# Kernel tuning notes

Measured on AMD Instinct MI355X. Metric: run time of the kernel, lower is better.

The kernel has to match this reference:

```python
import jax, jax.numpy as jnp
import numpy as np

E, T, H, I = 32, 512, 2048, 768


def setup_inputs() -> dict:
    key = jax.random.key(0)
    k1, k2, k3, k4 = jax.random.split(key, 4)
    scale = 1.0 / np.sqrt(H)
    return {
        "routed_input": jax.random.normal(k1, (E, T, H), dtype=jnp.float32),
        "gate_proj": jax.random.normal(k2, (E, I, H), dtype=jnp.float32) * scale,
        "up_proj": jax.random.normal(k3, (E, I, H), dtype=jnp.float32) * scale,
        "down_proj": jax.random.normal(k4, (E, H, I), dtype=jnp.float32) * scale,
    }


def reference(routed_input, gate_proj, up_proj, down_proj):
    # routed_input: [E, T, H]; per-expert SwiGLU MLP, concat over experts.
    gate = jnp.einsum("eth,eih->eti", routed_input, gate_proj)
    up = jnp.einsum("eth,eih->eti", routed_input, up_proj)
    hidden = jax.nn.silu(gate) * up  # [E, T, I]
    out = jnp.einsum("eti,ehi->eth", hidden, down_proj)  # [E, T, H]
    return out.reshape(E * T, H)
```

## Files before the change

kernel.cpp:

```cpp
#include <hip/hip_runtime.h>


#define NE 32
#define NT 512
#define NH 2048
#define NI 768

typedef short        short8  __attribute__((ext_vector_type(8)));
typedef float        floatx4 __attribute__((ext_vector_type(4)));
typedef __attribute__((address_space(1))) const unsigned int g_u32;
typedef __attribute__((address_space(3))) unsigned int l_u32;

__device__ __forceinline__ void gl_lds16(const void* g, void* l) {
    __builtin_amdgcn_global_load_lds((g_u32*)g, (l_u32*)l, 16, 0, 0);
}

__device__ __forceinline__ unsigned int cvt_pk_bf16(float lo, float hi) {
    unsigned int r;
    asm("v_cvt_pk_bf16_f32 %0, %1, %2" : "=v"(r) : "v"(lo), "v"(hi));
    return r;
}

__device__ __forceinline__ short8 frag8(floatx4 x0, floatx4 x1) {
    union { unsigned int u[4]; short8 s; } t;
    t.u[0] = cvt_pk_bf16(x0[0], x0[1]);
    t.u[1] = cvt_pk_bf16(x0[2], x0[3]);
    t.u[2] = cvt_pk_bf16(x1[0], x1[1]);
    t.u[3] = cvt_pk_bf16(x1[2], x1[3]);
    return t.s;
}

__device__ __forceinline__ ushort f2bf(float f) {
    union { float f; unsigned int u; } v; v.f = f;
    unsigned int r = v.u + 0x7fffu + ((v.u >> 16) & 1u);
    return (ushort)(r >> 16);
}

__global__ __launch_bounds__(256, 2) void moe_gateup(
    const float* __restrict__ rin, const float* __restrict__ gate,
    const float* __restrict__ up, ushort* __restrict__ hidden)
{
    __shared__ float As[128][32];
    __shared__ float Gs[128][32];
    __shared__ float Us[128][32];

    const int bid = blockIdx.x;
    const int wg  = (bid & 7) * (768 / 8) + (bid >> 3);
    const int e   = wg / 24;
    const int rem = wg % 24;
    const int ti  = rem % 6;
    const int tm  = rem / 6;

    const int tid  = threadIdx.x;
    const int lane = tid & 63;
    const int wave = tid >> 6;
    const int wr = wave >> 1, wc = wave & 1;

    const float* Ab = rin  + (size_t)e * NT * NH + (size_t)(tm * 128) * NH;
    const float* Gb = gate + (size_t)e * NI * NH + (size_t)(ti * 128) * NH;
    const float* Ub = up   + (size_t)e * NI * NH + (size_t)(ti * 128) * NH;

    const int lr = lane >> 3;
    const int lc = lane & 7;

    floatx4 accg[4][4], accu[4][4];
    #pragma unroll
    for (int m = 0; m < 4; ++m)
        #pragma unroll
        for (int n = 0; n < 4; ++n) {
            accg[m][n] = (floatx4)0.f;
            accu[m][n] = (floatx4)0.f;
        }

    const int frow = lane & 15;
    const int h    = lane >> 4;
    const int rb   = frow & 7;
    const int c0   = (2 * h) ^ rb;
    const int c1   = (2 * h + 1) ^ rb;
    const int KT = NH / 32;

    for (int kt = 0; kt < KT; ++kt) {
        const int k0 = kt * 32;
        __builtin_amdgcn_s_barrier();
        #pragma unroll
        for (int i = 0; i < 4; ++i) {
            const int g = wave * 4 + i;
            const int r = g * 8 + lr;
            const int cs = lc ^ (r & 7);
            const size_t so = (size_t)r * NH + k0 + cs * 4;
            gl_lds16(Ab + so, &As[g * 8][0]);
            gl_lds16(Gb + so, &Gs[g * 8][0]);
            gl_lds16(Ub + so, &Us[g * 8][0]);
        }
        asm volatile("s_waitcnt vmcnt(0)" ::: "memory");
        __builtin_amdgcn_s_barrier();

        short8 af[4], gf[4], uf[4];
        #pragma unroll
        for (int m = 0; m < 4; ++m) {
            const int R = wr * 64 + m * 16 + frow;
            af[m] = frag8(*(const floatx4*)&As[R][c0 * 4],
                          *(const floatx4*)&As[R][c1 * 4]);
        }
        #pragma unroll
        for (int n = 0; n < 4; ++n) {
            const int R = wc * 64 + n * 16 + frow;
            gf[n] = frag8(*(const floatx4*)&Gs[R][c0 * 4],
                          *(const floatx4*)&Gs[R][c1 * 4]);
            uf[n] = frag8(*(const floatx4*)&Us[R][c0 * 4],
                          *(const floatx4*)&Us[R][c1 * 4]);
        }
        #pragma unroll
        for (int m = 0; m < 4; ++m)
            #pragma unroll
            for (int n = 0; n < 4; ++n) {
                accg[m][n] = __builtin_amdgcn_mfma_f32_16x16x32_bf16(
                    af[m], gf[n], accg[m][n], 0, 0, 0);
                accu[m][n] = __builtin_amdgcn_mfma_f32_16x16x32_bf16(
                    af[m], uf[n], accu[m][n], 0, 0, 0);
            }
    }

    const int ccol  = lane & 15;
    const int crow0 = (lane >> 4) * 4;
    const size_t hbase = ((size_t)e * NT + (size_t)tm * 128) * NI + ti * 128;
    #pragma unroll
    for (int m = 0; m < 4; ++m)
        #pragma unroll
        for (int n = 0; n < 4; ++n)
            #pragma unroll
            for (int j = 0; j < 4; ++j) {
                const float g = accg[m][n][j];
                const float u = accu[m][n][j];
                const float hh = (g / (1.f + __expf(-g))) * u;
                const int row = wr * 64 + m * 16 + crow0 + j;
                const int col = wc * 64 + n * 16 + ccol;
                hidden[hbase + (size_t)row * NI + col] = f2bf(hh);
            }
}

__global__ __launch_bounds__(256, 2) void moe_down(
    const ushort* __restrict__ hidden, const float* __restrict__ down,
    float* __restrict__ out)
{
    __shared__ ushort As[128][32];
    __shared__ float  Bs[128][32];

    const int bid = blockIdx.x;
    const int wg  = (bid & 7) * (2048 / 8) + (bid >> 3);
    const int e   = wg >> 6;
    const int rem = wg & 63;
    const int tn  = rem & 15;
    const int tm  = rem >> 4;

    const int tid  = threadIdx.x;
    const int lane = tid & 63;
    const int wave = tid >> 6;
    const int wr = wave >> 1, wc = wave & 1;

    const ushort* Ab = hidden + ((size_t)e * NT + (size_t)tm * 128) * NI;
    const float*  Bb = down + (size_t)e * NH * NI + (size_t)(tn * 128) * NI;

    floatx4 acc[4][4];
    #pragma unroll
    for (int m = 0; m < 4; ++m)
        #pragma unroll
        for (int n = 0; n < 4; ++n) acc[m][n] = (floatx4)0.f;

    const int frow = lane & 15;
    const int h    = lane >> 4;
    const int ca   = h ^ (frow & 3);
    const int rb   = frow & 7;
    const int c0   = (2 * h) ^ rb;
    const int c1   = (2 * h + 1) ^ rb;
    const int KT = NI / 32;

    for (int kt = 0; kt < KT; ++kt) {
        const int k0 = kt * 32;
        __builtin_amdgcn_s_barrier();
        #pragma unroll
        for (int i = 0; i < 2; ++i) {
            const int g = wave * 2 + i;
            const int r = g * 16 + (lane >> 2);
            const int cs = (lane & 3) ^ (r & 3);
            gl_lds16(Ab + (size_t)r * NI + k0 + cs * 8, &As[g * 16][0]);
        }
        #pragma unroll
        for (int i = 0; i < 4; ++i) {
            const int g = wave * 4 + i;
            const int r = g * 8 + (lane >> 3);
            const int cs = (lane & 7) ^ (r & 7);
            gl_lds16(Bb + (size_t)r * NI + k0 + cs * 4, &Bs[g * 8][0]);
        }
        asm volatile("s_waitcnt vmcnt(0)" ::: "memory");
        __builtin_amdgcn_s_barrier();

        short8 af[4], bf[4];
        #pragma unroll
        for (int m = 0; m < 4; ++m) {
            const int R = wr * 64 + m * 16 + frow;
            af[m] = *(const short8*)&As[R][ca * 8];
        }
        #pragma unroll
        for (int n = 0; n < 4; ++n) {
            const int R = wc * 64 + n * 16 + frow;
            bf[n] = frag8(*(const floatx4*)&Bs[R][c0 * 4],
                          *(const floatx4*)&Bs[R][c1 * 4]);
        }
        #pragma unroll
        for (int m = 0; m < 4; ++m)
            #pragma unroll
            for (int n = 0; n < 4; ++n)
                acc[m][n] = __builtin_amdgcn_mfma_f32_16x16x32_bf16(
                    af[m], bf[n], acc[m][n], 0, 0, 0);
    }

    const int ccol  = lane & 15;
    const int crow0 = (lane >> 4) * 4;
    float* Ob = out + ((size_t)e * NT + (size_t)tm * 128) * NH + tn * 128;
    #pragma unroll
    for (int m = 0; m < 4; ++m)
        #pragma unroll
        for (int n = 0; n < 4; ++n)
            #pragma unroll
            for (int j = 0; j < 4; ++j) {
                const int row = wr * 64 + m * 16 + crow0 + j;
                const int col = wc * 64 + n * 16 + ccol;
                Ob[(size_t)row * NH + col] = acc[m][n][j];
            }
}

extern "C" void kernel_launch(void* const* d_in, const int* in_sizes, int n_in,
                              void* d_out, int out_size, void* d_ws, size_t ws_size,
                              hipStream_t stream) {
    const float* rin  = (const float*)d_in[0];
    const float* gate = (const float*)d_in[1];
    const float* up   = (const float*)d_in[2];
    const float* down = (const float*)d_in[3];
    float* out = (float*)d_out;
    ushort* hidden = (ushort*)d_ws;

    dim3 blk(256);
    moe_gateup<<<dim3(768), blk, 0, stream>>>(rin, gate, up, hidden);
    moe_down<<<dim3(2048), blk, 0, stream>>>(hidden, down, out);
}
```

Before: 384.0 us.

## Double-buffer LDS tiles in gate/up and down GEMM kernels

Both GEMM kernels now keep two LDS buffers and issue the global-to-LDS loads for the next K tile before computing on the current one. They wait only for the older batch with a partial vmcnt and add a trailing barrier so the buffer being refilled is no longer being read. The aim is to hide global load latency behind MFMA work instead of fully serialising load and compute. In exchange, LDS use doubles (96KB for gate/up), and gate/up's launch bound drops to one block per CU, which lowers occupancy.

```diff
diff --git a/kernel.cpp b/kernel.cpp
--- a/kernel.cpp
+++ b/kernel.cpp
@@ -36,13 +36,13 @@
     return (ushort)(r >> 16);
 }
 
-__global__ __launch_bounds__(256, 2) void moe_gateup(
+__global__ __launch_bounds__(256, 1) void moe_gateup(
     const float* __restrict__ rin, const float* __restrict__ gate,
     const float* __restrict__ up, ushort* __restrict__ hidden)
 {
-    __shared__ float As[128][32];
-    __shared__ float Gs[128][32];
-    __shared__ float Us[128][32];
+    __shared__ float As[2][128][32];
+    __shared__ float Gs[2][128][32];
+    __shared__ float Us[2][128][32];
 
     const int bid = blockIdx.x;
     const int wg  = (bid & 7) * (768 / 8) + (bid >> 3);
@@ -79,36 +79,46 @@
     const int c1   = (2 * h + 1) ^ rb;
     const int KT = NH / 32;
 
+#define STAGE_GU(kt, b) do {                                                 \
+        const int k0_ = (kt) * 32;                                           \
+        _Pragma("unroll")                                                    \
+        for (int i = 0; i < 4; ++i) {                                        \
+            const int g_ = wave * 4 + i;                                     \
+            const int r_ = g_ * 8 + lr;                                      \
+            const int cs_ = lc ^ (r_ & 7);                                   \
+            const size_t so_ = (size_t)r_ * NH + k0_ + cs_ * 4;              \
+            gl_lds16(Ab + so_, &As[b][g_ * 8][0]);                           \
+            gl_lds16(Gb + so_, &Gs[b][g_ * 8][0]);                           \
+            gl_lds16(Ub + so_, &Us[b][g_ * 8][0]);                           \
+        }                                                                    \
+    } while (0)
+
+    STAGE_GU(0, 0);
+
     for (int kt = 0; kt < KT; ++kt) {
-        const int k0 = kt * 32;
-        __builtin_amdgcn_s_barrier();
-        #pragma unroll
-        for (int i = 0; i < 4; ++i) {
-            const int g = wave * 4 + i;
-            const int r = g * 8 + lr;
-            const int cs = lc ^ (r & 7);
-            const size_t so = (size_t)r * NH + k0 + cs * 4;
-            gl_lds16(Ab + so, &As[g * 8][0]);
-            gl_lds16(Gb + so, &Gs[g * 8][0]);
-            gl_lds16(Ub + so, &Us[g * 8][0]);
-        }
-        asm volatile("s_waitcnt vmcnt(0)" ::: "memory");
+        const int cur = kt & 1;
+        if (kt + 1 < KT) {
+            STAGE_GU(kt + 1, cur ^ 1);
+            asm volatile("s_waitcnt vmcnt(12)" ::: "memory");
+        } else {
+            asm volatile("s_waitcnt vmcnt(0)" ::: "memory");
+        }
         __builtin_amdgcn_s_barrier();
 
         short8 af[4], gf[4], uf[4];
         #pragma unroll
         for (int m = 0; m < 4; ++m) {
             const int R = wr * 64 + m * 16 + frow;
-            af[m] = frag8(*(const floatx4*)&As[R][c0 * 4],
-                          *(const floatx4*)&As[R][c1 * 4]);
+            af[m] = frag8(*(const floatx4*)&As[cur][R][c0 * 4],
+                          *(const floatx4*)&As[cur][R][c1 * 4]);
         }
         #pragma unroll
         for (int n = 0; n < 4; ++n) {
             const int R = wc * 64 + n * 16 + frow;
-            gf[n] = frag8(*(const floatx4*)&Gs[R][c0 * 4],
-                          *(const floatx4*)&Gs[R][c1 * 4]);
-            uf[n] = frag8(*(const floatx4*)&Us[R][c0 * 4],
-                          *(const floatx4*)&Us[R][c1 * 4]);
+            gf[n] = frag8(*(const floatx4*)&Gs[cur][R][c0 * 4],
+                          *(const floatx4*)&Gs[cur][R][c1 * 4]);
+            uf[n] = frag8(*(const floatx4*)&Us[cur][R][c0 * 4],
+                          *(const floatx4*)&Us[cur][R][c1 * 4]);
         }
         #pragma unroll
         for (int m = 0; m < 4; ++m)
@@ -119,7 +129,12 @@
                 accu[m][n] = __builtin_amdgcn_mfma_f32_16x16x32_bf16(
                     af[m], uf[n], accu[m][n], 0, 0, 0);
             }
+
+        asm volatile("s_waitcnt lgkmcnt(0)" ::: "memory");
+        __builtin_amdgcn_sched_barrier(0);
+        __builtin_amdgcn_s_barrier();
     }
+#undef STAGE_GU
 
     const int ccol  = lane & 15;
     const int crow0 = (lane >> 4) * 4;
@@ -143,8 +158,8 @@
     const ushort* __restrict__ hidden, const float* __restrict__ down,
     float* __restrict__ out)
 {
-    __shared__ ushort As[128][32];
-    __shared__ float  Bs[128][32];
+    __shared__ ushort As[2][128][32];
+    __shared__ float  Bs[2][128][32];
 
     const int bid = blockIdx.x;
     const int wg  = (bid & 7) * (2048 / 8) + (bid >> 3);
@@ -175,37 +190,47 @@
     const int c1   = (2 * h + 1) ^ rb;
     const int KT = NI / 32;
 
+#define STAGE_DN(kt, b) do {                                                 \
+        const int k0_ = (kt) * 32;                                           \
+        _Pragma("unroll")                                                    \
+        for (int i = 0; i < 2; ++i) {                                        \
+            const int g_ = wave * 2 + i;                                     \
+            const int r_ = g_ * 16 + (lane >> 2);                            \
+            const int cs_ = (lane & 3) ^ (r_ & 3);                           \
+            gl_lds16(Ab + (size_t)r_ * NI + k0_ + cs_ * 8, &As[b][g_ * 16][0]); \
+        }                                                                    \
+        _Pragma("unroll")                                                    \
+        for (int i = 0; i < 4; ++i) {                                        \
+            const int g_ = wave * 4 + i;                                     \
+            const int r_ = g_ * 8 + (lane >> 3);                             \
+            const int cs_ = (lane & 7) ^ (r_ & 7);                           \
+            gl_lds16(Bb + (size_t)r_ * NI + k0_ + cs_ * 4, &Bs[b][g_ * 8][0]); \
+        }                                                                    \
+    } while (0)
+
+    STAGE_DN(0, 0);
+
     for (int kt = 0; kt < KT; ++kt) {
-        const int k0 = kt * 32;
-        __builtin_amdgcn_s_barrier();
-        #pragma unroll
-        for (int i = 0; i < 2; ++i) {
-            const int g = wave * 2 + i;
-            const int r = g * 16 + (lane >> 2);
-            const int cs = (lane & 3) ^ (r & 3);
-            gl_lds16(Ab + (size_t)r * NI + k0 + cs * 8, &As[g * 16][0]);
-        }
-        #pragma unroll
-        for (int i = 0; i < 4; ++i) {
-            const int g = wave * 4 + i;
-            const int r = g * 8 + (lane >> 3);
-            const int cs = (lane & 7) ^ (r & 7);
-            gl_lds16(Bb + (size_t)r * NI + k0 + cs * 4, &Bs[g * 8][0]);
-        }
-        asm volatile("s_waitcnt vmcnt(0)" ::: "memory");
+        const int cur = kt & 1;
+        if (kt + 1 < KT) {
+            STAGE_DN(kt + 1, cur ^ 1);
+            asm volatile("s_waitcnt vmcnt(6)" ::: "memory");
+        } else {
+            asm volatile("s_waitcnt vmcnt(0)" ::: "memory");
+        }
         __builtin_amdgcn_s_barrier();
 
         short8 af[4], bf[4];
         #pragma unroll
         for (int m = 0; m < 4; ++m) {
             const int R = wr * 64 + m * 16 + frow;
-            af[m] = *(const short8*)&As[R][ca * 8];
+            af[m] = *(const short8*)&As[cur][R][ca * 8];
         }
         #pragma unroll
         for (int n = 0; n < 4; ++n) {
             const int R = wc * 64 + n * 16 + frow;
-            bf[n] = frag8(*(const floatx4*)&Bs[R][c0 * 4],
-                          *(const floatx4*)&Bs[R][c1 * 4]);
+            bf[n] = frag8(*(const floatx4*)&Bs[cur][R][c0 * 4],
+                          *(const floatx4*)&Bs[cur][R][c1 * 4]);
         }
         #pragma unroll
         for (int m = 0; m < 4; ++m)
@@ -213,7 +238,12 @@
             for (int n = 0; n < 4; ++n)
                 acc[m][n] = __builtin_amdgcn_mfma_f32_16x16x32_bf16(
                     af[m], bf[n], acc[m][n], 0, 0, 0);
+
+        asm volatile("s_waitcnt lgkmcnt(0)" ::: "memory");
+        __builtin_amdgcn_sched_barrier(0);
+        __builtin_amdgcn_s_barrier();
     }
+#undef STAGE_DN
 
     const int ccol  = lane & 15;
     const int crow0 = (lane >> 4) * 4;
```

New measurement: 494.1 us. +28.7%, slower.
